# Optimization experiments

Hardware: AMD Instinct MI355X
Metric: run time of the kernel (lower is better)

## Reference

```python
import jax, jax.numpy as jnp
import numpy as np

M = 15   # state dim
N = 15   # obs dim
H = M * M  # 225, GRU hidden dims


def _lin(x, W, b):
    return x @ W.T + b


def _gru_cell(x, h, Wih, Whh, bih, bhh):
    # PyTorch nn.GRU cell math. x:[B,In], h:[B,H]
    gi = x @ Wih.T + bih
    gh = h @ Whh.T + bhh
    i_r, i_z, i_n = jnp.split(gi, 3, axis=-1)
    h_r, h_z, h_n = jnp.split(gh, 3, axis=-1)
    r = jax.nn.sigmoid(i_r + h_r)
    z = jax.nn.sigmoid(i_z + h_z)
    n = jnp.tanh(i_n + r * h_n)
    return (1.0 - z) * n + z * h


def setup_inputs() -> dict:
    key = jax.random.key(0)
    ks = iter(jax.random.split(key, 64))
    T, B = 256, 16

    def w(shape):
        fan_in = shape[-1]
        return (jax.random.uniform(next(ks), shape, jnp.float32, -1.0, 1.0)
                / np.sqrt(fan_in).astype(np.float32))

    inp = {
        "y": jax.random.normal(next(ks), (T, B, 30), jnp.float32),
        "x0": jax.random.normal(next(ks), (B, M), jnp.float32),
        "hQ0": jax.random.normal(next(ks), (B, H), jnp.float32) * 0.1,
        "hSig0": jax.random.normal(next(ks), (B, H), jnp.float32) * 0.1,
        "hS0": jax.random.normal(next(ks), (B, H), jnp.float32) * 0.1,
    }
    # GRUs: Q (in 75), Sigma (in 300), S (in 375), hidden 225 each
    for name, ind in (("Q", M * 5), ("Sig", H + M * 5), ("S", N * N + 2 * N * 5)):
        inp[f"Wih{name}"] = w((3 * H, ind))
        inp[f"Whh{name}"] = w((3 * H, H))
        inp[f"bih{name}"] = jnp.zeros((3 * H,), jnp.float32)
        inp[f"bhh{name}"] = jnp.zeros((3 * H,), jnp.float32)
    # FC stack
    hid2 = (2 * H) * 40  # 18000
    inp["W1"] = w((N * N, H)); inp["b1"] = jnp.zeros((N * N,), jnp.float32)
    inp["W2a"] = w((hid2, 2 * H)); inp["b2a"] = jnp.zeros((hid2,), jnp.float32)
    inp["W2b"] = w((N * M, hid2)); inp["b2b"] = jnp.zeros((N * M,), jnp.float32)
    inp["W3"] = w((M * M, H + N * M)); inp["b3"] = jnp.zeros((M * M,), jnp.float32)
    inp["W4"] = w((H, H + M * M)); inp["b4"] = jnp.zeros((H,), jnp.float32)
    inp["W5"] = w((M * 5, M)); inp["b5"] = jnp.zeros((M * 5,), jnp.float32)
    inp["W6"] = w((M * 5, M)); inp["b6"] = jnp.zeros((M * 5,), jnp.float32)
    inp["W7"] = w((2 * N * 5, 2 * N)); inp["b7"] = jnp.zeros((2 * N * 5,), jnp.float32)
    return inp


def _knet_forward(y, x0, hQ0, hSig0, hS0,
                  WihQ, WhhQ, bihQ, bhhQ,
                  WihSig, WhhSig, bihSig, bhhSig,
                  WihS, WhhS, bihS, bhhS,
                  W1, b1, W2a, b2a, W2b, b2b, W3, b3, W4, b4,
                  W5, b5, W6, b6, W7, b7):
    relu = jax.nn.relu
    B = x0.shape[0]

    def step(carry, y_t):
        x_post, x_post_prev, x_prior_prev, y_prev, hQ, hSig, hS = carry
        obs = y_t[:, :N]                      # y[:15]
        # SysModel.f / h stand-in: identity dynamics (system model is external)
        x_prior = x_post
        y_hat = x_prior
        # KGain_Step difference features
        obs_diff = obs - y_prev
        obs_innov_diff = obs - y_hat
        fw_evol_diff = x_post - x_post_prev
        fw_update_diff = x_post - x_prior_prev
        # KGain chain
        out5 = relu(_lin(fw_evol_diff, W5, b5))
        hQ = _gru_cell(out5, hQ, WihQ, WhhQ, bihQ, bhhQ)
        out6 = relu(_lin(fw_update_diff, W6, b6))
        out_sigma = _gru_cell(jnp.concatenate([hQ, out6], -1), hSig,
                              WihSig, WhhSig, bihSig, bhhSig)
        out1 = relu(_lin(out_sigma, W1, b1))
        out7 = relu(_lin(jnp.concatenate([obs_diff, obs_innov_diff], -1), W7, b7))
        hS = _gru_cell(jnp.concatenate([out1, out7], -1), hS,
                       WihS, WhhS, bihS, bhhS)
        out2 = _lin(relu(_lin(jnp.concatenate([out_sigma, hS], -1), W2a, b2a)), W2b, b2b)
        out3 = relu(_lin(jnp.concatenate([hS, out2], -1), W3, b3))
        out4 = relu(_lin(jnp.concatenate([out_sigma, out3], -1), W4, b4))
        hSig = out4                            # h_Sigma <- FC4 output (as in source)
        KG = out2.reshape(B, M, N)
        dy = obs - y_hat                       # [B, N]
        # faithful to `(x_prior + KG*dy)[0]`: row 0 of broadcasted sum
        x_post_new = x_prior + KG[:, 0, :] * dy
        new_carry = (x_post_new, x_post, x_prior, obs, hQ, hSig, hS)
        return new_carry, x_post_new

    init = (x0, x0, x0, x0, hQ0, hSig0, hS0)   # y_prev = h(x0) = x0
    _, xs = jax.lax.scan(step, init, y)
    return xs  # [T, B, M]


def reference(y, x0, hQ0, hSig0, hS0,
              WihQ, WhhQ, bihQ, bhhQ,
              WihSig, WhhSig, bihSig, bhhSig,
              WihS, WhhS, bihS, bhhS,
              W1, b1, W2a, b2a, W2b, b2b, W3, b3, W4, b4,
              W5, b5, W6, b6, W7, b7):
    return _knet_forward(y, x0, hQ0, hSig0, hS0,
                         WihQ, WhhQ, bihQ, bhhQ,
                         WihSig, WhhSig, bihSig, bhhSig,
                         WihS, WhhS, bihS, bhhS,
                         W1, b1, W2a, b2a, W2b, b2b, W3, b3, W4, b4,
                         W5, b5, W6, b6, W7, b7)
```

## Files before the change

kernel.cpp:

```cpp
#include <hip/hip_runtime.h>
#include <math.h>


#define NWG 256
#define NTH 1024
#define TT  256
#define NEPOCH 1792
#define EP_STRIDE 272
#define OFF_GO   (NEPOCH*EP_STRIDE)
#define INT_TOTAL (OFF_GO + 16)

#define F_HQ    0
#define F_HS    7296
#define F_HSIG  14592
#define F_XP    18240
#define F_DY    18480
#define F_FWD   18736
#define F_OBSD  18992
#define F_OSIG  19248
#define F_OUT1  22896
#define F_OUT3  26544
#define F_XV    30192
#define F_OUT2  37424
#define F_HID2  52016
#define PQ      340016
#define PSIG    545216
#define PS      912416
#define PW1     1322816
#define PW3     1374116
#define PW4     1476716
#define PW5     1579316
#define PW6     1580516
#define PW7     1581716
#define W2AP    1586516

#define L_OUT5 0
#define L_OUT6 1216
#define L_OUT7 2432
#define L_OUT2 4864
#define L_XV   0
#define L_SCR  8512
#define L_TOTAL 18000

typedef float v4f __attribute__((ext_vector_type(4)));

struct KArgs {
  const float *y,*x0,*hQ0,*hSig0,*hS0;
  const float *WihQ,*WhhQ,*bihQ,*bhhQ;
  const float *WihSig,*WhhSig,*bihSig,*bhhSig;
  const float *WihS,*WhhS,*bihS,*bhhS;
  const float *W1,*b1,*W2a,*b2a,*W2b,*b2b,*W3,*b3,*W4,*b4;
  const float *W5,*b5,*W6,*b6,*W7,*b7;
  float* out;
  int*   ib;
  float* fb;
};

__device__ __forceinline__ float sigf(float x) { return 1.0f/(1.0f + __expf(-x)); }
__device__ __forceinline__ float dp4(float acc, float4 w, float4 x) {
  acc = fmaf(w.x, x.x, acc); acc = fmaf(w.y, x.y, acc);
  acc = fmaf(w.z, x.z, acc); acc = fmaf(w.w, x.w, acc);
  return acc;
}
__device__ __forceinline__ float4 ldg4(const float* p){ return *(const float4*)p; }

__device__ __forceinline__ float ald(const float* p) {
  return __hip_atomic_load(p, __ATOMIC_RELAXED, __HIP_MEMORY_SCOPE_AGENT);
}
__device__ __forceinline__ float4 ald4(const float* p) {
  float4 r; r.x=ald(p); r.y=ald(p+1); r.z=ald(p+2); r.w=ald(p+3); return r;
}
__device__ __forceinline__ void ast(float* p, float v) {
  __hip_atomic_store(p, v, __ATOMIC_RELAXED, __HIP_MEMORY_SCOPE_AGENT);
}
__device__ __forceinline__ void aadd(float* p, float v) {
  __hip_atomic_fetch_add(p, v, __ATOMIC_RELAXED, __HIP_MEMORY_SCOPE_AGENT);
}

__device__ __forceinline__ float red64(float v) {
  v += __shfl_xor(v, 1, 64);  v += __shfl_xor(v, 2, 64);
  v += __shfl_xor(v, 4, 64);  v += __shfl_xor(v, 8, 64);
  v += __shfl_xor(v, 16, 64); v += __shfl_xor(v, 32, 64);
  return v;
}

__device__ __forceinline__ void gbar(int* ib, int e) {
  __builtin_amdgcn_s_waitcnt(0);
  __syncthreads();
  if (threadIdx.x == 0) {
    const int base = e * EP_STRIDE;
    const int g = (int)(blockIdx.x >> 4);
    int prev = __hip_atomic_fetch_add(ib + base + g*16, 1,
                                      __ATOMIC_RELAXED, __HIP_MEMORY_SCOPE_AGENT);
    if (prev == 15) {
      int pt = __hip_atomic_fetch_add(ib + base + 256, 1,
                                      __ATOMIC_RELAXED, __HIP_MEMORY_SCOPE_AGENT);
      if (pt == 15)
        __hip_atomic_store(ib + OFF_GO, e, __ATOMIC_RELAXED, __HIP_MEMORY_SCOPE_AGENT);
    }
    while (__hip_atomic_load(ib + OFF_GO, __ATOMIC_RELAXED, __HIP_MEMORY_SCOPE_AGENT) < e)
      __builtin_amdgcn_s_sleep(2);
  }
  __syncthreads();
}

__global__ void knet_init(KArgs a) {
  int gt = blockIdx.x*blockDim.x + threadIdx.x;
  int nt = gridDim.x*blockDim.x;
  float* F = a.fb;
  for (int i = gt; i < INT_TOTAL; i += nt) a.ib[i] = (i == OFF_GO) ? -1 : 0;
  for (int i = gt; i < 3648; i += nt) {
    int b = i/228, j = i - b*228;
    float hq=0.f, hs=0.f, hg=0.f;
    if (j < 225) { hq = a.hQ0[b*225+j]; hs = a.hS0[b*225+j]; hg = a.hSig0[b*225+j]; }
    F[F_HQ + i] = hq; F[F_HS + i] = hs; F[F_HSIG + i] = hg;
    F[F_OSIG + i] = 0.f; F[F_OUT3 + i] = 0.f; F[F_OUT1 + i] = 0.f;
    F[F_OUT2 + i] = 0.f;
  }
  for (int i = gt; i < 7232; i += nt) F[F_XV + i] = 0.f;
  for (int i = gt; i < 240; i += nt) F[F_XP + i] = a.x0[i];
  for (int i = gt; i < 256; i += nt) {
    int b = i >> 4, j = i & 15;
    float dy=0.f, od=0.f;
    if (j < 15) {
      float ob = a.y[b*30 + j], xv = a.x0[b*15 + j];
      dy = ob - xv; od = ob - xv;
    }
    F[F_DY + i] = dy; F[F_OBSD + i] = od; F[F_FWD + i] = 0.f;
  }
  for (int i = gt; i < 675*304; i += nt) {
    int r = i/304, d = i - r*304; float v = 0.f;
    if (d < 75) v = a.WihQ[r*75 + d];
    else if (d >= 76 && d < 301) v = a.WhhQ[r*225 + d - 76];
    F[PQ + i] = v;
  }
  for (int i = gt; i < 675*544; i += nt) {
    int r = i/544, d = i - r*544; float v = 0.f;
    if (d < 225) v = a.WihSig[r*300 + d];
    else if (d >= 228 && d < 303) v = a.WihSig[r*300 + 225 + d - 228];
    else if (d >= 304 && d < 529) v = a.WhhSig[r*225 + d - 304];
    F[PSIG + i] = v;
  }
  for (int i = gt; i < 675*608; i += nt) {
    int r = i/608, d = i - r*608; float v = 0.f;
    if (d < 225) v = a.WihS[r*375 + d];
    else if (d >= 228 && d < 378) v = a.WihS[r*375 + 225 + d - 228];
    else if (d >= 380 && d < 605) v = a.WhhS[r*225 + d - 380];
    F[PS + i] = v;
  }
  for (int i = gt; i < 225*228; i += nt) {
    int r = i/228, d = i - r*228;
    F[PW1 + i] = (d < 225) ? a.W1[r*225 + d] : 0.f;
  }
  for (int i = gt; i < 225*456; i += nt) {
    int r = i/456, d = i - r*456; float v3 = 0.f, v4 = 0.f;
    if (d < 225)               { v3 = a.W3[r*450 + d];           v4 = a.W4[r*450 + d]; }
    else if (d >= 228 && d < 453) { v3 = a.W3[r*450 + 225 + d - 228]; v4 = a.W4[r*450 + 225 + d - 228]; }
    F[PW3 + i] = v3; F[PW4 + i] = v4;
  }
  for (int i = gt; i < 75*16; i += nt) {
    int r = i >> 4, d = i & 15;
    F[PW5 + i] = (d < 15) ? a.W5[r*15 + d] : 0.f;
    F[PW6 + i] = (d < 15) ? a.W6[r*15 + d] : 0.f;
  }
  for (int i = gt; i < 150*32; i += nt) {
    int r = i >> 5, d = i & 31; float v = 0.f;
    if (d < 15) v = a.W7[r*30 + d];
    else if (d >= 16 && d < 31) v = a.W7[r*30 + 15 + d - 16];
    F[PW7 + i] = v;
  }
  for (long long i = gt; i < 18000LL*452; i += nt) {
    long long r = i/452; int d = (int)(i - r*452);
    F[W2AP + i] = (d < 450) ? a.W2a[r*450 + d] : 0.f;
  }
}

__global__ __launch_bounds__(NTH, 4) void knet_main(KArgs a) {
  __shared__ float smem[L_TOTAL];
  const int tid  = threadIdx.x;
  const int widx = tid >> 6;
  const int l    = tid & 63;
  const int bx   = (int)blockIdx.x;
  const int k0   = l*4;
  float* F  = a.fb;
  int*   ib = a.ib;
  int ep = 0;

  for (int t = 0; t < TT; ++t) {
    const int p = t & 1, q = p ^ 1;
    float* hQi = F + F_HQ + p*3648;  float* hQo = F + F_HQ + q*3648;
    float* hSi = F + F_HS + p*3648;  float* hSo = F + F_HS + q*3648;

    if (bx < 225) {
      if (tid < 256) smem[L_SCR + tid] = ald(F + F_FWD + tid);
      __syncthreads();
      for (int i = tid; i < 1200; i += NTH) {
        int bb = i/75, j5 = i - bb*75;
        const float4* w  = (const float4*)(F + PW5 + j5*16);
        const float4* xv = (const float4*)(smem + L_SCR + bb*16);
        float acc = a.b5[j5];
        acc = dp4(acc, w[0], xv[0]); acc = dp4(acc, w[1], xv[1]);
        acc = dp4(acc, w[2], xv[2]); acc = dp4(acc, w[3], xv[3]);
        smem[L_OUT5 + bb*76 + j5] = fmaxf(acc, 0.f);
      }
      __syncthreads();
      const int j = bx, bw = widx;
      float4 xq0 = (k0 < 76) ? *(const float4*)(smem + L_OUT5 + bw*76 + k0)
                             : ald4(hQi + bw*228 + k0 - 76);
      float4 xq1; if (l < 12) xq1 = ald4(hQi + bw*228 + 180 + k0);
      float4 xw0 = (l < 57) ? ald4(F + F_OSIG + bw*228 + k0)
                            : ald4(F + F_OUT3 + bw*228 + k0 - 228);
      float4 xw1; if (l < 50) xw1 = ald4(F + F_OUT3 + bw*228 + 28 + k0);
      const float* qr = F + PQ + (size_t)j*304;
      const float* qz = qr + 225*304;
      const float* qn = qr + 450*304;
      const float* w4r = F + PW4 + (size_t)j*456;
      float4 wr0 = ldg4(qr + k0), wz0 = ldg4(qz + k0), wn0 = ldg4(qn + k0);
      float4 w40 = ldg4(w4r + k0);
      float ar=0.f, az=0.f, ani=0.f, anh=0.f, a4=0.f;
      ar = dp4(ar, wr0, xq0); az = dp4(az, wz0, xq0);
      { float tt = dp4(0.f, wn0, xq0); if (k0 < 76) ani += tt; else anh += tt; }
      a4 = dp4(a4, w40, xw0);
      if (l < 12) {
        float4 wr1 = ldg4(qr + 256 + k0), wz1 = ldg4(qz + 256 + k0), wn1 = ldg4(qn + 256 + k0);
        ar = dp4(ar, wr1, xq1); az = dp4(az, wz1, xq1); anh = dp4(anh, wn1, xq1);
      }
      if (l < 50) a4 = dp4(a4, ldg4(w4r + 256 + k0), xw1);
      ar = red64(ar); az = red64(az); ani = red64(ani); anh = red64(anh); a4 = red64(a4);
      if (l == 0) {
        float r = sigf(ar + a.bihQ[j] + a.bhhQ[j]);
        float z = sigf(az + a.bihQ[225+j] + a.bhhQ[225+j]);
        float n = tanhf(ani + a.bihQ[450+j] + r*(anh + a.bhhQ[450+j]));
        ast(&hQo[bw*228 + j], (1.f - z)*n + z*ald(&hQi[bw*228 + j]));
        if (t > 0) ast(&F[F_HSIG + bw*228 + j], fmaxf(a4 + a.b4[j], 0.f));
      }
    } else if (bx == 225) {
      for (int i = tid; i < 3648; i += NTH) ast(&F[F_OUT2 + i], 0.f);
    }
    gbar(ib, ep); ++ep;

    if (bx < 225) {
      for (int i = tid; i < 1200; i += NTH) {
        int bb = i/75, j6 = i - bb*75;
        const float4* w  = (const float4*)(F + PW6 + j6*16);
        const float4* xv = (const float4*)(smem + L_SCR + bb*16);
        float acc = a.b6[j6];
        acc = dp4(acc, w[0], xv[0]); acc = dp4(acc, w[1], xv[1]);
        acc = dp4(acc, w[2], xv[2]); acc = dp4(acc, w[3], xv[3]);
        smem[L_OUT6 + bb*76 + j6] = fmaxf(acc, 0.f);
      }
      __syncthreads();
      const int j = bx, bw = widx;
      float4 x0 = (l < 57) ? ald4(hQo + bw*228 + k0)
                           : *(const float4*)(smem + L_OUT6 + bw*76 + k0 - 228);
      float4 x1 = (l < 12) ? *(const float4*)(smem + L_OUT6 + bw*76 + 28 + k0)
                           : ald4(F + F_HSIG + bw*228 + k0 - 48);
      float4 x2; if (l < 5) x2 = ald4(F + F_HSIG + bw*228 + 208 + k0);
      const float* gr = F + PSIG + (size_t)j*544;
      const float* gz = gr + 225*544;
      const float* gn = gr + 450*544;
      float4 wr0 = ldg4(gr + k0),     wz0 = ldg4(gz + k0),     wn0 = ldg4(gn + k0);
      float4 wr1 = ldg4(gr + 256+k0), wz1 = ldg4(gz + 256+k0), wn1 = ldg4(gn + 256+k0);
      float ar=0.f, az=0.f, ani=0.f, anh=0.f;
      ar = dp4(ar, wr0, x0); az = dp4(az, wz0, x0); ani = dp4(ani, wn0, x0);
      ar = dp4(ar, wr1, x1); az = dp4(az, wz1, x1);
      { float tt = dp4(0.f, wn1, x1); if (l < 12) ani += tt; else anh += tt; }
      if (l < 5) {
        float4 wr2 = ldg4(gr + 512+k0), wz2 = ldg4(gz + 512+k0), wn2 = ldg4(gn + 512+k0);
        ar = dp4(ar, wr2, x2); az = dp4(az, wz2, x2); anh = dp4(anh, wn2, x2);
      }
      ar = red64(ar); az = red64(az); ani = red64(ani); anh = red64(anh);
      if (l == 0) {
        float r = sigf(ar + a.bihSig[j] + a.bhhSig[j]);
        float z = sigf(az + a.bihSig[225+j] + a.bhhSig[225+j]);
        float n = tanhf(ani + a.bihSig[450+j] + r*(anh + a.bhhSig[450+j]));
        float val = (1.f - z)*n + z*ald(&F[F_HSIG + bw*228 + j]);
        ast(&F[F_OSIG + bw*228 + j], val);
        ast(&F[F_XV + bw*452 + j], val);
      }
    }
    gbar(ib, ep); ++ep;

    if (bx < 225) {
      const int j = bx, bw = widx;
      float acc = 0.f;
      if (l < 57) {
        float4 w0 = ldg4(F + PW1 + (size_t)j*228 + k0);
        float4 x0 = ald4(F + F_OSIG + bw*228 + k0);
        acc = dp4(0.f, w0, x0);
      }
      acc = red64(acc);
      if (l == 0) ast(&F[F_OUT1 + bw*228 + j], fmaxf(acc + a.b1[j], 0.f));
    }
    gbar(ib, ep); ++ep;

    if (bx < 225) {
      if (tid < 256)      smem[L_SCR + tid]       = ald(F + F_OBSD + tid);
      else if (tid < 512) smem[L_SCR + tid]       = ald(F + F_DY + tid - 256);
      __syncthreads();
      for (int i = tid; i < 2400; i += NTH) {
        int bb = i/150, j7 = i - bb*150;
        const float4* w  = (const float4*)(F + PW7 + j7*32);
        const float4* vo = (const float4*)(smem + L_SCR + bb*16);
        const float4* vd = (const float4*)(smem + L_SCR + 256 + bb*16);
        float acc = a.b7[j7];
        acc = dp4(acc, w[0], vo[0]); acc = dp4(acc, w[1], vo[1]);
        acc = dp4(acc, w[2], vo[2]); acc = dp4(acc, w[3], vo[3]);
        acc = dp4(acc, w[4], vd[0]); acc = dp4(acc, w[5], vd[1]);
        acc = dp4(acc, w[6], vd[2]); acc = dp4(acc, w[7], vd[3]);
        smem[L_OUT7 + bb*152 + j7] = fmaxf(acc, 0.f);
      }
      __syncthreads();
      const int j = bx, bw = widx;
      float4 x0 = (l < 57) ? ald4(F + F_OUT1 + bw*228 + k0)
                           : *(const float4*)(smem + L_OUT7 + bw*152 + k0 - 228);
      float4 x1 = (l < 31) ? *(const float4*)(smem + L_OUT7 + bw*152 + 28 + k0)
                           : ald4(hSi + bw*228 + k0 - 124);
      float4 x2; if (l < 24) x2 = ald4(hSi + bw*228 + 132 + k0);
      const float* gr = F + PS + (size_t)j*608;
      const float* gz = gr + 225*608;
      const float* gn = gr + 450*608;
      float4 wr0 = ldg4(gr + k0),     wz0 = ldg4(gz + k0),     wn0 = ldg4(gn + k0);
      float4 wr1 = ldg4(gr + 256+k0), wz1 = ldg4(gz + 256+k0), wn1 = ldg4(gn + 256+k0);
      float ar=0.f, az=0.f, ani=0.f, anh=0.f;
      ar = dp4(ar, wr0, x0); az = dp4(az, wz0, x0); ani = dp4(ani, wn0, x0);
      ar = dp4(ar, wr1, x1); az = dp4(az, wz1, x1);
      { float tt = dp4(0.f, wn1, x1); if (l < 31) ani += tt; else anh += tt; }
      if (l < 24) {
        float4 wr2 = ldg4(gr + 512+k0), wz2 = ldg4(gz + 512+k0), wn2 = ldg4(gn + 512+k0);
        ar = dp4(ar, wr2, x2); az = dp4(az, wz2, x2); anh = dp4(anh, wn2, x2);
      }
      ar = red64(ar); az = red64(az); ani = red64(ani); anh = red64(anh);
      if (l == 0) {
        float r = sigf(ar + a.bihS[j] + a.bhhS[j]);
        float z = sigf(az + a.bihS[225+j] + a.bhhS[225+j]);
        float n = tanhf(ani + a.bihS[450+j] + r*(anh + a.bhhS[450+j]));
        float val = (1.f - z)*n + z*ald(&hSi[bw*228 + j]);
        ast(&hSo[bw*228 + j], val);
        ast(&F[F_XV + bw*452 + 225 + j], val);
      }
    }
    gbar(ib, ep); ++ep;

    {
      for (int i = tid; i < 7232; i += NTH) smem[L_XV + i] = ald(F + F_XV + i);
      __syncthreads();
      if (bx < 250) {
        const int r0 = bx*72;
        for (int ps = 0; ps < 3; ++ps) {
          const int pi = ps*16 + widx;
          if (pi >= 36) break;
          const int rA = r0 + 2*pi;
          const float* wAp = F + W2AP + (size_t)rA*452;
          const float* wBp = wAp + 452;
          float aA[16], aB[16];
          #pragma unroll
          for (int i = 0; i < 16; ++i) { aA[i] = 0.f; aB[i] = 0.f; }
          {
            float4 wA = ldg4(wAp + k0), wB = ldg4(wBp + k0);
            #pragma unroll
            for (int bb = 0; bb < 16; ++bb) {
              float4 xv = *(const float4*)(smem + L_XV + bb*452 + k0);
              aA[bb] = dp4(aA[bb], wA, xv);
              aB[bb] = dp4(aB[bb], wB, xv);
            }
          }
          if (l < 49) {
            float4 wA = ldg4(wAp + 256 + k0), wB = ldg4(wBp + 256 + k0);
            #pragma unroll
            for (int bb = 0; bb < 16; ++bb) {
              float4 xv = *(const float4*)(smem + L_XV + bb*452 + 256 + k0);
              aA[bb] = dp4(aA[bb], wA, xv);
              aB[bb] = dp4(aB[bb], wB, xv);
            }
          }
          #pragma unroll
          for (int i = 0; i < 16; ++i) { aA[i] = red64(aA[i]); aB[i] = red64(aB[i]); }
          if (l == 0) {
            float bA = a.b2a[rA], bB = a.b2a[rA + 1];
            #pragma unroll
            for (int i = 0; i < 16; ++i) {
              ast(&F[F_HID2 + i*18000 + rA],     fmaxf(aA[i] + bA, 0.f));
              ast(&F[F_HID2 + i*18000 + rA + 1], fmaxf(aB[i] + bB, 0.f));
            }
          }
        }
      }
    }
    gbar(ib, ep); ++ep;

    if (bx < 225) {
      const int jt = bx / 45, kc = bx - jt*45;
      const int j0 = jt*45, col0 = kc*400;
      const int b = widx;
      const float* hb = F + F_HID2 + (size_t)b*18000 + col0;
      float4 h0 = ald4(hb + 4*l);
      float4 h1; if (l < 36) h1 = ald4(hb + 256 + 4*l);
      for (int idx = tid; idx < 4500; idx += NTH) {
        int jj = idx / 100, cc = idx - jj*100;
        *(float4*)(smem + jj*400 + cc*4) =
            ldg4(a.W2b + (size_t)(j0+jj)*18000 + col0 + cc*4);
      }
      __syncthreads();
      #pragma unroll 5
      for (int jj = 0; jj < 45; ++jj) {
        const float* wrow = smem + jj*400;
        float acc = dp4(0.f, *(const float4*)(wrow + 4*l), h0);
        if (l < 36) acc = dp4(acc, *(const float4*)(wrow + 256 + 4*l), h1);
        acc = red64(acc);
        if (l == 0) aadd(&F[F_OUT2 + b*228 + j0 + jj], acc);
      }
    }
    gbar(ib, ep); ++ep;

    if (bx < 225) {
      for (int i = tid; i < 3648; i += NTH) {
        int bb = i/228, j2 = i - bb*228;
        float v = 0.f;
        if (j2 < 225) v = ald(&F[F_OUT2 + i]) + a.b2b[j2];
        smem[L_OUT2 + i] = v;
      }
      __syncthreads();
      const int j = bx, bw = widx;
      float4 x0 = (l < 57) ? ald4(hSo + bw*228 + k0)
                           : *(const float4*)(smem + L_OUT2 + bw*228 + k0 - 228);
      float4 x1; if (l < 50) x1 = *(const float4*)(smem + L_OUT2 + bw*228 + 28 + k0);
      const float* w3r = F + PW3 + (size_t)j*456;
      float acc = dp4(0.f, ldg4(w3r + k0), x0);
      if (l < 50) acc = dp4(acc, ldg4(w3r + 256 + k0), x1);
      acc = red64(acc);
      if (l == 0) ast(&F[F_OUT3 + bw*228 + j], fmaxf(acc + a.b3[j], 0.f));
    } else if (bx == 225) {
      for (int i = tid; i < 240; i += NTH) {
        int bb = i/15, jj = i - bb*15;
        float o2 = ald(&F[F_OUT2 + bb*228 + jj]) + a.b2b[jj];
        float xold = ald(&F[F_XP + i]), dy = ald(&F[F_DY + bb*16 + jj]);
        float xnew = fmaf(o2, dy, xold);
        a.out[t*240 + i] = xnew;
        ast(&F[F_XP + i], xnew);
        if (t + 1 < TT) {
          float y1 = a.y[(t+1)*480 + bb*30 + jj];
          float y0 = a.y[t*480     + bb*30 + jj];
          ast(&F[F_DY   + bb*16 + jj], y1 - xnew);
          ast(&F[F_OBSD + bb*16 + jj], y1 - y0);
          ast(&F[F_FWD  + bb*16 + jj], xnew - xold);
        }
      }
    }
    gbar(ib, ep); ++ep;
  }
}

extern "C" void kernel_launch(void* const* d_in, const int* in_sizes, int n_in,
                              void* d_out, int out_size, void* d_ws, size_t ws_size,
                              hipStream_t stream) {
  (void)in_sizes; (void)n_in; (void)out_size; (void)ws_size;
  KArgs a;
  int k = 0;
  a.y      = (const float*)d_in[k++];
  a.x0     = (const float*)d_in[k++];
  a.hQ0    = (const float*)d_in[k++];
  a.hSig0  = (const float*)d_in[k++];
  a.hS0    = (const float*)d_in[k++];
  a.WihQ   = (const float*)d_in[k++];
  a.WhhQ   = (const float*)d_in[k++];
  a.bihQ   = (const float*)d_in[k++];
  a.bhhQ   = (const float*)d_in[k++];
  a.WihSig = (const float*)d_in[k++];
  a.WhhSig = (const float*)d_in[k++];
  a.bihSig = (const float*)d_in[k++];
  a.bhhSig = (const float*)d_in[k++];
  a.WihS   = (const float*)d_in[k++];
  a.WhhS   = (const float*)d_in[k++];
  a.bihS   = (const float*)d_in[k++];
  a.bhhS   = (const float*)d_in[k++];
  a.W1  = (const float*)d_in[k++];  a.b1  = (const float*)d_in[k++];
  a.W2a = (const float*)d_in[k++];  a.b2a = (const float*)d_in[k++];
  a.W2b = (const float*)d_in[k++];  a.b2b = (const float*)d_in[k++];
  a.W3  = (const float*)d_in[k++];  a.b3  = (const float*)d_in[k++];
  a.W4  = (const float*)d_in[k++];  a.b4  = (const float*)d_in[k++];
  a.W5  = (const float*)d_in[k++];  a.b5  = (const float*)d_in[k++];
  a.W6  = (const float*)d_in[k++];  a.b6  = (const float*)d_in[k++];
  a.W7  = (const float*)d_in[k++];  a.b7  = (const float*)d_in[k++];
  a.out = (float*)d_out;
  a.ib  = (int*)d_ws;
  a.fb  = (float*)((char*)d_ws + (size_t)INT_TOTAL*sizeof(int));

  hipLaunchKernelGGL(knet_init, dim3(2048), dim3(256), 0, stream, a);
  hipLaunchKernelGGL(knet_main, dim3(NWG), dim3(NTH), 0, stream, a);
}
```

Measured before the change: 29.95 ms.

## Keep each block's W2a slice resident in LDS across all timesteps

Each of the 250 blocks loads its 72-row slice of the padded W2a weight (about 130KB) into shared memory once before the time loop, and the hidden-layer matmul then reads weights from LDS instead of global/L2 every step. To fit, the LDS layout is rearranged: the other per-phase scratch regions move after the resident weights, and the W2b tile staging is split into three chunks of 15 rows. This removes roughly 32MB of weight traffic per timestep. In exchange, shared memory per block grows to about 159KB, which limits occupancy to one 1024-thread block per CU, and the W2b phase gains extra block-level syncs.

Result: slower. 30.62 ms (+2.2%).

```diff
diff --git a/kernel.cpp b/kernel.cpp
--- a/kernel.cpp
+++ b/kernel.cpp
@@ -34,13 +34,17 @@
 #define PW7     1581716
 #define W2AP    1586516
 
-#define L_OUT5 0
-#define L_OUT6 1216
-#define L_OUT7 2432
-#define L_OUT2 4864
-#define L_XV   0
-#define L_SCR  8512
-#define L_TOTAL 18000
+#define LW2A    0
+#define S0      32544
+#define LA_OUT5 (S0)
+#define LA_OUT6 (S0+1216)
+#define LAB_SCR (S0+2432)
+#define LD_OUT7 (S0)
+#define LD_SCR  (S0+2432)
+#define LE_XV   (S0)
+#define LF_W2B  (S0)
+#define LG_OUT2 (S0)
+#define L_TOTAL 39776
 
 typedef float v4f __attribute__((ext_vector_type(4)));
 
@@ -186,26 +190,33 @@
   int*   ib = a.ib;
   int ep = 0;
 
+  if (bx < 250) {
+    const float* src = F + W2AP + (size_t)bx*72*452;
+    for (int i = tid; i < 8136; i += NTH)
+      *(float4*)(smem + LW2A + i*4) = ldg4(src + i*4);
+  }
+  __syncthreads();
+
   for (int t = 0; t < TT; ++t) {
     const int p = t & 1, q = p ^ 1;
     float* hQi = F + F_HQ + p*3648;  float* hQo = F + F_HQ + q*3648;
     float* hSi = F + F_HS + p*3648;  float* hSo = F + F_HS + q*3648;
 
     if (bx < 225) {
-      if (tid < 256) smem[L_SCR + tid] = ald(F + F_FWD + tid);
+      if (tid < 256) smem[LAB_SCR + tid] = ald(F + F_FWD + tid);
       __syncthreads();
       for (int i = tid; i < 1200; i += NTH) {
         int bb = i/75, j5 = i - bb*75;
         const float4* w  = (const float4*)(F + PW5 + j5*16);
-        const float4* xv = (const float4*)(smem + L_SCR + bb*16);
+        const float4* xv = (const float4*)(smem + LAB_SCR + bb*16);
         float acc = a.b5[j5];
         acc = dp4(acc, w[0], xv[0]); acc = dp4(acc, w[1], xv[1]);
         acc = dp4(acc, w[2], xv[2]); acc = dp4(acc, w[3], xv[3]);
-        smem[L_OUT5 + bb*76 + j5] = fmaxf(acc, 0.f);
+        smem[LA_OUT5 + bb*76 + j5] = fmaxf(acc, 0.f);
       }
       __syncthreads();
       const int j = bx, bw = widx;
-      float4 xq0 = (k0 < 76) ? *(const float4*)(smem + L_OUT5 + bw*76 + k0)
+      float4 xq0 = (k0 < 76) ? *(const float4*)(smem + LA_OUT5 + bw*76 + k0)
                              : ald4(hQi + bw*228 + k0 - 76);
       float4 xq1; if (l < 12) xq1 = ald4(hQi + bw*228 + 180 + k0);
       float4 xw0 = (l < 57) ? ald4(F + F_OSIG + bw*228 + k0)
@@ -243,17 +254,17 @@
       for (int i = tid; i < 1200; i += NTH) {
         int bb = i/75, j6 = i - bb*75;
         const float4* w  = (const float4*)(F + PW6 + j6*16);
-        const float4* xv = (const float4*)(smem + L_SCR + bb*16);
+        const float4* xv = (const float4*)(smem + LAB_SCR + bb*16);
         float acc = a.b6[j6];
         acc = dp4(acc, w[0], xv[0]); acc = dp4(acc, w[1], xv[1]);
         acc = dp4(acc, w[2], xv[2]); acc = dp4(acc, w[3], xv[3]);
-        smem[L_OUT6 + bb*76 + j6] = fmaxf(acc, 0.f);
+        smem[LA_OUT6 + bb*76 + j6] = fmaxf(acc, 0.f);
       }
       __syncthreads();
       const int j = bx, bw = widx;
       float4 x0 = (l < 57) ? ald4(hQo + bw*228 + k0)
-                           : *(const float4*)(smem + L_OUT6 + bw*76 + k0 - 228);
-      float4 x1 = (l < 12) ? *(const float4*)(smem + L_OUT6 + bw*76 + 28 + k0)
+                           : *(const float4*)(smem + LA_OUT6 + bw*76 + k0 - 228);
+      float4 x1 = (l < 12) ? *(const float4*)(smem + LA_OUT6 + bw*76 + 28 + k0)
                            : ald4(F + F_HSIG + bw*228 + k0 - 48);
       float4 x2; if (l < 5) x2 = ald4(F + F_HSIG + bw*228 + 208 + k0);
       const float* gr = F + PSIG + (size_t)j*544;
@@ -295,26 +306,26 @@
     gbar(ib, ep); ++ep;
 
     if (bx < 225) {
-      if (tid < 256)      smem[L_SCR + tid]       = ald(F + F_OBSD + tid);
-      else if (tid < 512) smem[L_SCR + tid]       = ald(F + F_DY + tid - 256);
+      if (tid < 256)      smem[LD_SCR + tid]       = ald(F + F_OBSD + tid);
+      else if (tid < 512) smem[LD_SCR + tid]       = ald(F + F_DY + tid - 256);
       __syncthreads();
       for (int i = tid; i < 2400; i += NTH) {
         int bb = i/150, j7 = i - bb*150;
         const float4* w  = (const float4*)(F + PW7 + j7*32);
-        const float4* vo = (const float4*)(smem + L_SCR + bb*16);
-        const float4* vd = (const float4*)(smem + L_SCR + 256 + bb*16);
+        const float4* vo = (const float4*)(smem + LD_SCR + bb*16);
+        const float4* vd = (const float4*)(smem + LD_SCR + 256 + bb*16);
         float acc = a.b7[j7];
         acc = dp4(acc, w[0], vo[0]); acc = dp4(acc, w[1], vo[1]);
         acc = dp4(acc, w[2], vo[2]); acc = dp4(acc, w[3], vo[3]);
         acc = dp4(acc, w[4], vd[0]); acc = dp4(acc, w[5], vd[1]);
         acc = dp4(acc, w[6], vd[2]); acc = dp4(acc, w[7], vd[3]);
-        smem[L_OUT7 + bb*152 + j7] = fmaxf(acc, 0.f);
+        smem[LD_OUT7 + bb*152 + j7] = fmaxf(acc, 0.f);
       }
       __syncthreads();
       const int j = bx, bw = widx;
       float4 x0 = (l < 57) ? ald4(F + F_OUT1 + bw*228 + k0)
-                           : *(const float4*)(smem + L_OUT7 + bw*152 + k0 - 228);
-      float4 x1 = (l < 31) ? *(const float4*)(smem + L_OUT7 + bw*152 + 28 + k0)
+                           : *(const float4*)(smem + LD_OUT7 + bw*152 + k0 - 228);
+      float4 x1 = (l < 31) ? *(const float4*)(smem + LD_OUT7 + bw*152 + 28 + k0)
                            : ald4(hSi + bw*228 + k0 - 124);
       float4 x2; if (l < 24) x2 = ald4(hSi + bw*228 + 132 + k0);
       const float* gr = F + PS + (size_t)j*608;
@@ -343,33 +354,36 @@
     gbar(ib, ep); ++ep;
 
     {
-      for (int i = tid; i < 7232; i += NTH) smem[L_XV + i] = ald(F + F_XV + i);
+      for (int i = tid; i < 7232; i += NTH) smem[LE_XV + i] = ald(F + F_XV + i);
       __syncthreads();
       if (bx < 250) {
         const int r0 = bx*72;
         for (int ps = 0; ps < 3; ++ps) {
           const int pi = ps*16 + widx;
           if (pi >= 36) break;
-          const int rA = r0 + 2*pi;
-          const float* wAp = F + W2AP + (size_t)rA*452;
+          const int lr = 2*pi;
+          const int rA = r0 + lr;
+          const float* wAp = smem + LW2A + lr*452;
           const float* wBp = wAp + 452;
           float aA[16], aB[16];
           #pragma unroll
           for (int i = 0; i < 16; ++i) { aA[i] = 0.f; aB[i] = 0.f; }
           {
-            float4 wA = ldg4(wAp + k0), wB = ldg4(wBp + k0);
+            float4 wA = *(const float4*)(wAp + k0);
+            float4 wB = *(const float4*)(wBp + k0);
             #pragma unroll
             for (int bb = 0; bb < 16; ++bb) {
-              float4 xv = *(const float4*)(smem + L_XV + bb*452 + k0);
+              float4 xv = *(const float4*)(smem + LE_XV + bb*452 + k0);
               aA[bb] = dp4(aA[bb], wA, xv);
               aB[bb] = dp4(aB[bb], wB, xv);
             }
           }
           if (l < 49) {
-            float4 wA = ldg4(wAp + 256 + k0), wB = ldg4(wBp + 256 + k0);
+            float4 wA = *(const float4*)(wAp + 256 + k0);
+            float4 wB = *(const float4*)(wBp + 256 + k0);
             #pragma unroll
             for (int bb = 0; bb < 16; ++bb) {
-              float4 xv = *(const float4*)(smem + L_XV + bb*452 + 256 + k0);
+              float4 xv = *(const float4*)(smem + LE_XV + bb*452 + 256 + k0);
               aA[bb] = dp4(aA[bb], wA, xv);
               aB[bb] = dp4(aB[bb], wB, xv);
             }
@@ -396,19 +410,22 @@
       const float* hb = F + F_HID2 + (size_t)b*18000 + col0;
       float4 h0 = ald4(hb + 4*l);
       float4 h1; if (l < 36) h1 = ald4(hb + 256 + 4*l);
-      for (int idx = tid; idx < 4500; idx += NTH) {
-        int jj = idx / 100, cc = idx - jj*100;
-        *(float4*)(smem + jj*400 + cc*4) =
-            ldg4(a.W2b + (size_t)(j0+jj)*18000 + col0 + cc*4);
-      }
-      __syncthreads();
-      #pragma unroll 5
-      for (int jj = 0; jj < 45; ++jj) {
-        const float* wrow = smem + jj*400;
-        float acc = dp4(0.f, *(const float4*)(wrow + 4*l), h0);
-        if (l < 36) acc = dp4(acc, *(const float4*)(wrow + 256 + 4*l), h1);
-        acc = red64(acc);
-        if (l == 0) aadd(&F[F_OUT2 + b*228 + j0 + jj], acc);
+      for (int c0 = 0; c0 < 45; c0 += 15) {
+        __syncthreads();
+        for (int idx = tid; idx < 1500; idx += NTH) {
+          int jj = idx / 100, cc = idx - jj*100;
+          *(float4*)(smem + LF_W2B + jj*400 + cc*4) =
+              ldg4(a.W2b + (size_t)(j0+c0+jj)*18000 + col0 + cc*4);
+        }
+        __syncthreads();
+        #pragma unroll 5
+        for (int jj = 0; jj < 15; ++jj) {
+          const float* wrow = smem + LF_W2B + jj*400;
+          float acc = dp4(0.f, *(const float4*)(wrow + 4*l), h0);
+          if (l < 36) acc = dp4(acc, *(const float4*)(wrow + 256 + 4*l), h1);
+          acc = red64(acc);
+          if (l == 0) aadd(&F[F_OUT2 + b*228 + j0 + c0 + jj], acc);
+        }
       }
     }
     gbar(ib, ep); ++ep;
@@ -418,13 +435,13 @@
         int bb = i/228, j2 = i - bb*228;
         float v = 0.f;
         if (j2 < 225) v = ald(&F[F_OUT2 + i]) + a.b2b[j2];
-        smem[L_OUT2 + i] = v;
+        smem[LG_OUT2 + i] = v;
       }
       __syncthreads();
       const int j = bx, bw = widx;
       float4 x0 = (l < 57) ? ald4(hSo + bw*228 + k0)
-                           : *(const float4*)(smem + L_OUT2 + bw*228 + k0 - 228);
-      float4 x1; if (l < 50) x1 = *(const float4*)(smem + L_OUT2 + bw*228 + 28 + k0);
+                           : *(const float4*)(smem + LG_OUT2 + bw*228 + k0 - 228);
+      float4 x1; if (l < 50) x1 = *(const float4*)(smem + LG_OUT2 + bw*228 + 28 + k0);
       const float* w3r = F + PW3 + (size_t)j*456;
       float acc = dp4(0.f, ldg4(w3r + k0), x0);
       if (l < 50) acc = dp4(acc, ldg4(w3r + 256 + k0), x1);
```
